# Performance work log

Hardware: AMD Instinct MI355X
Metric: run time of the kernel (lower is better)

## Reference

```python
import jax, jax.numpy as jnp
import numpy as np

N = 100_000      # nodes
E = 1_600_000    # edges (avg degree 16)
D_IN = 64
D_OUT = 64


def setup_inputs() -> dict:
    key = jax.random.key(0)
    k_x, k_row, k_ptr, k_w, k_b = jax.random.split(key, 5)
    x = jax.random.normal(k_x, (N, D_IN), dtype=jnp.float32)
    # CSC graph: row = source node index per edge, colptr = per-target-node edge offsets
    row = jax.random.randint(k_row, (E,), 0, N, dtype=jnp.int32)
    inner = jnp.sort(jax.random.randint(k_ptr, (N - 1,), 0, E, dtype=jnp.int32))
    colptr = jnp.concatenate([jnp.zeros((1,), jnp.int32), inner,
                              jnp.full((1,), E, jnp.int32)])
    # Linear(2*in_channels -> out_channels) weights, torch layout [out, in]
    W = jax.random.normal(k_w, (D_OUT, 2 * D_IN), dtype=jnp.float32) * 0.05
    b = jax.random.normal(k_b, (D_OUT,), dtype=jnp.float32) * 0.05
    return {"x": x, "row": row, "colptr": colptr, "W": W, "b": b}


def reference(x, row, colptr, W, b):
    num_nodes = x.shape[0]
    num_edges = row.shape[0]
    # Recover per-edge target node id from colptr (CSC -> COO col)
    col = jnp.searchsorted(colptr, jnp.arange(num_edges, dtype=colptr.dtype),
                           side='right') - 1  # [E]
    # Mean aggregation of neighbor (source) features onto target nodes
    gathered = x[row]                                             # [E, D_IN]
    summed = jax.ops.segment_sum(gathered, col, num_segments=num_nodes)
    deg = (colptr[1:] - colptr[:-1]).astype(x.dtype)              # [N]
    agg = summed / jnp.clip(deg, 1.0)[:, None]                    # [N, D_IN]
    # SAGEConvAgg output = concat(agg_neighbors, root features); then Linear
    feat = jnp.concatenate([agg, x], axis=-1)                     # [N, 2*D_IN]
    return feat @ W.T + b                                         # [N, D_OUT]
```

## Files before the change

### kernel.cpp

```cpp
#include <hip/hip_runtime.h>

typedef __bf16 bf16x8 __attribute__((ext_vector_type(8)));
typedef float  f32x4  __attribute__((ext_vector_type(4)));

__device__ __forceinline__ unsigned short f2bf(float f) {
  unsigned u = __float_as_uint(f);
  u = u + 0x7fffu + ((u >> 16) & 1u);
  return (unsigned short)(u >> 16);
}
__device__ __forceinline__ float bf2f(unsigned short h) {
  return __uint_as_float(((unsigned)h) << 16);
}

__global__ __launch_bounds__(256) void cvt_bf16(
    const float* __restrict__ x, unsigned short* __restrict__ xb, int total8) {
  int i = blockIdx.x * 256 + threadIdx.x;
  if (i >= total8) return;
  const float4* p = (const float4*)(x + (size_t)i * 8);
  float4 a = p[0], b = p[1];
  union { unsigned short u[8]; uint4 v; } r;
  r.u[0] = f2bf(a.x); r.u[1] = f2bf(a.y); r.u[2] = f2bf(a.z); r.u[3] = f2bf(a.w);
  r.u[4] = f2bf(b.x); r.u[5] = f2bf(b.y); r.u[6] = f2bf(b.z); r.u[7] = f2bf(b.w);
  ((uint4*)xb)[i] = r.v;
}

template <bool BF>
__global__ __launch_bounds__(256) void sage_agg(
    const float* __restrict__ x, const unsigned short* __restrict__ xb,
    const int* __restrict__ row, const int* __restrict__ colptr,
    float* __restrict__ agg, int N) {
  int wid  = blockIdx.x * 4 + (threadIdx.x >> 6);
  int lane = threadIdx.x & 63;
  if (wid >= N) return;
  int s = colptr[wid], e = colptr[wid + 1];
  float acc = 0.0f;
  int t = s;
#define LDX(r) (BF ? bf2f(xb[(size_t)(r) * 64 + lane]) : x[(size_t)(r) * 64 + lane])
  for (; t + 8 <= e; t += 8) {
    int r0 = row[t],     r1 = row[t + 1], r2 = row[t + 2], r3 = row[t + 3];
    int r4 = row[t + 4], r5 = row[t + 5], r6 = row[t + 6], r7 = row[t + 7];
    float v0 = LDX(r0), v1 = LDX(r1), v2 = LDX(r2), v3 = LDX(r3);
    float v4 = LDX(r4), v5 = LDX(r5), v6 = LDX(r6), v7 = LDX(r7);
    acc += ((v0 + v1) + (v2 + v3)) + ((v4 + v5) + (v6 + v7));
  }
  for (; t + 4 <= e; t += 4) {
    int r0 = row[t], r1 = row[t + 1], r2 = row[t + 2], r3 = row[t + 3];
    float v0 = LDX(r0), v1 = LDX(r1), v2 = LDX(r2), v3 = LDX(r3);
    acc += (v0 + v1) + (v2 + v3);
  }
  for (; t < e; ++t) acc += LDX(row[t]);
#undef LDX
  int deg = e - s;
  agg[(size_t)wid * 64 + lane] = (deg > 0) ? (acc / (float)deg) : 0.0f;
}

template <bool BF>
__global__ __launch_bounds__(256) void sage_mm(
    const float* __restrict__ x, const unsigned short* __restrict__ xb,
    const float* __restrict__ W, const float* __restrict__ b,
    float* __restrict__ out, int N) {
  __shared__ unsigned short ft[128][136];
  int tid = threadIdx.x;
  int l = tid & 63, w = tid >> 6;
  int colr = l & 15, kg = l >> 4;
  int n0 = blockIdx.x * 128;
  int rows = N - n0; if (rows > 128) rows = 128;

  bf16x8 bfrag[4][4];
  float bias[4];
  #pragma unroll
  for (int c = 0; c < 4; ++c) {
    bias[c] = b[c * 16 + colr];
    #pragma unroll
    for (int kq = 0; kq < 4; ++kq) {
      const float* wp = W + (size_t)(c * 16 + colr) * 128 + kq * 32 + kg * 8;
      float4 wa = *(const float4*)wp;
      float4 wb = *(const float4*)(wp + 4);
      union { unsigned short u[8]; bf16x8 v; } r;
      r.u[0] = f2bf(wa.x); r.u[1] = f2bf(wa.y); r.u[2] = f2bf(wa.z); r.u[3] = f2bf(wa.w);
      r.u[4] = f2bf(wb.x); r.u[5] = f2bf(wb.y); r.u[6] = f2bf(wb.z); r.u[7] = f2bf(wb.w);
      bfrag[c][kq] = r.v;
    }
  }

  const float* aggsrc = out + (size_t)n0 * 64;
  #pragma unroll
  for (int it = 0; it < 4; ++it) {
    int flat = it * 2048 + tid * 8;
    int n = flat >> 6, k = flat & 63;
    {
      union { unsigned short u[8]; uint4 v; } r;
      if (n < rows) {
        const float4* p = (const float4*)(aggsrc + (size_t)n * 64 + k);
        float4 a = p[0], bb = p[1];
        r.u[0] = f2bf(a.x);  r.u[1] = f2bf(a.y);  r.u[2] = f2bf(a.z);  r.u[3] = f2bf(a.w);
        r.u[4] = f2bf(bb.x); r.u[5] = f2bf(bb.y); r.u[6] = f2bf(bb.z); r.u[7] = f2bf(bb.w);
      } else { r.v = make_uint4(0, 0, 0, 0); }
      *(uint4*)&ft[n][k] = r.v;
    }
    {
      uint4 v;
      if (BF) {
        v = (n < rows) ? *(const uint4*)(xb + ((size_t)(n0 + n) * 64 + k))
                       : make_uint4(0, 0, 0, 0);
      } else {
        union { unsigned short u[8]; uint4 vv; } r;
        if (n < rows) {
          const float4* p = (const float4*)(x + (size_t)(n0 + n) * 64 + k);
          float4 a = p[0], bb = p[1];
          r.u[0] = f2bf(a.x);  r.u[1] = f2bf(a.y);  r.u[2] = f2bf(a.z);  r.u[3] = f2bf(a.w);
          r.u[4] = f2bf(bb.x); r.u[5] = f2bf(bb.y); r.u[6] = f2bf(bb.z); r.u[7] = f2bf(bb.w);
        } else { r.vv = make_uint4(0, 0, 0, 0); }
        v = r.vv;
      }
      *(uint4*)&ft[n][64 + k] = v;
    }
  }
  __syncthreads();

  f32x4 acc[2][4];
  #pragma unroll
  for (int m = 0; m < 2; ++m)
    #pragma unroll
    for (int c = 0; c < 4; ++c)
      acc[m][c] = (f32x4){bias[c], bias[c], bias[c], bias[c]};

  #pragma unroll
  for (int kq = 0; kq < 4; ++kq) {
    bf16x8 a0 = *(const bf16x8*)&ft[w * 32 + colr][kq * 32 + kg * 8];
    bf16x8 a1 = *(const bf16x8*)&ft[w * 32 + 16 + colr][kq * 32 + kg * 8];
    #pragma unroll
    for (int c = 0; c < 4; ++c) {
      acc[0][c] = __builtin_amdgcn_mfma_f32_16x16x32_bf16(a0, bfrag[c][kq], acc[0][c], 0, 0, 0);
      acc[1][c] = __builtin_amdgcn_mfma_f32_16x16x32_bf16(a1, bfrag[c][kq], acc[1][c], 0, 0, 0);
    }
  }

  #pragma unroll
  for (int m = 0; m < 2; ++m) {
    int nodeb = n0 + w * 32 + m * 16 + kg * 4;
    #pragma unroll
    for (int c = 0; c < 4; ++c) {
      #pragma unroll
      for (int r = 0; r < 4; ++r) {
        int node = nodeb + r;
        if (node < N) out[(size_t)node * 64 + c * 16 + colr] = acc[m][c][r];
      }
    }
  }
}

extern "C" void kernel_launch(void* const* d_in, const int* in_sizes, int n_in,
                              void* d_out, int out_size, void* d_ws, size_t ws_size,
                              hipStream_t stream) {
  const float* x      = (const float*)d_in[0];
  const int*   row    = (const int*)d_in[1];
  const int*   colptr = (const int*)d_in[2];
  const float* W      = (const float*)d_in[3];
  const float* b      = (const float*)d_in[4];
  float* out = (float*)d_out;

  int N = in_sizes[0] / 64;
  bool bf = ws_size >= (size_t)N * 64 * sizeof(unsigned short);
  unsigned short* xb = (unsigned short*)d_ws;

  if (bf) {
    int total8 = N * 8;
    cvt_bf16<<<(total8 + 255) / 256, 256, 0, stream>>>(x, xb, total8);
    sage_agg<true><<<(N + 3) / 4, 256, 0, stream>>>(x, xb, row, colptr, out, N);
    sage_mm<true><<<(N + 127) / 128, 256, 0, stream>>>(x, xb, W, b, out, N);
  } else {
    sage_agg<false><<<(N + 3) / 4, 256, 0, stream>>>(x, xb, row, colptr, out, N);
    sage_mm<false><<<(N + 127) / 128, 256, 0, stream>>>(x, xb, W, b, out, N);
  }
}
```

Before: 94.71 us.

## Fuse neighbor aggregation into the MFMA linear kernel via shared memory

Merges the separate aggregation and matmul kernels into one: each wave gathers and averages neighbor features for 32 nodes and writes the bf16 result straight into the shared tile used by the MFMA product. This removes the fp32 round trip of the aggregated features through global memory and one kernel launch. In exchange, the gather runs with far fewer waves (one block per 128 nodes, each wave looping serially over nodes), which reduces the memory-level parallelism available to hide random gather latency. The edge loop is unrolled to 16 to compensate.

```diff
diff --git a/kernel.cpp b/kernel.cpp
--- a/kernel.cpp
+++ b/kernel.cpp
@@ -25,105 +25,79 @@
 }
 
 template <bool BF>
-__global__ __launch_bounds__(256) void sage_agg(
+__global__ __launch_bounds__(256, 4) void sage_fused(
     const float* __restrict__ x, const unsigned short* __restrict__ xb,
     const int* __restrict__ row, const int* __restrict__ colptr,
-    float* __restrict__ agg, int N) {
-  int wid  = blockIdx.x * 4 + (threadIdx.x >> 6);
-  int lane = threadIdx.x & 63;
-  if (wid >= N) return;
-  int s = colptr[wid], e = colptr[wid + 1];
-  float acc = 0.0f;
-  int t = s;
-#define LDX(r) (BF ? bf2f(xb[(size_t)(r) * 64 + lane]) : x[(size_t)(r) * 64 + lane])
-  for (; t + 8 <= e; t += 8) {
-    int r0 = row[t],     r1 = row[t + 1], r2 = row[t + 2], r3 = row[t + 3];
-    int r4 = row[t + 4], r5 = row[t + 5], r6 = row[t + 6], r7 = row[t + 7];
-    float v0 = LDX(r0), v1 = LDX(r1), v2 = LDX(r2), v3 = LDX(r3);
-    float v4 = LDX(r4), v5 = LDX(r5), v6 = LDX(r6), v7 = LDX(r7);
-    acc += ((v0 + v1) + (v2 + v3)) + ((v4 + v5) + (v6 + v7));
-  }
-  for (; t + 4 <= e; t += 4) {
-    int r0 = row[t], r1 = row[t + 1], r2 = row[t + 2], r3 = row[t + 3];
-    float v0 = LDX(r0), v1 = LDX(r1), v2 = LDX(r2), v3 = LDX(r3);
-    acc += (v0 + v1) + (v2 + v3);
-  }
-  for (; t < e; ++t) acc += LDX(row[t]);
-#undef LDX
-  int deg = e - s;
-  agg[(size_t)wid * 64 + lane] = (deg > 0) ? (acc / (float)deg) : 0.0f;
-}
-
-template <bool BF>
-__global__ __launch_bounds__(256) void sage_mm(
-    const float* __restrict__ x, const unsigned short* __restrict__ xb,
-    const float* __restrict__ W, const float* __restrict__ b,
+    const float* __restrict__ W, const float* __restrict__ bias,
     float* __restrict__ out, int N) {
   __shared__ unsigned short ft[128][136];
   int tid = threadIdx.x;
   int l = tid & 63, w = tid >> 6;
-  int colr = l & 15, kg = l >> 4;
   int n0 = blockIdx.x * 128;
   int rows = N - n0; if (rows > 128) rows = 128;
 
-  bf16x8 bfrag[4][4];
-  float bias[4];
-  #pragma unroll
-  for (int c = 0; c < 4; ++c) {
-    bias[c] = b[c * 16 + colr];
-    #pragma unroll
-    for (int kq = 0; kq < 4; ++kq) {
-      const float* wp = W + (size_t)(c * 16 + colr) * 128 + kq * 32 + kg * 8;
-      float4 wa = *(const float4*)wp;
-      float4 wb = *(const float4*)(wp + 4);
-      union { unsigned short u[8]; bf16x8 v; } r;
-      r.u[0] = f2bf(wa.x); r.u[1] = f2bf(wa.y); r.u[2] = f2bf(wa.z); r.u[3] = f2bf(wa.w);
-      r.u[4] = f2bf(wb.x); r.u[5] = f2bf(wb.y); r.u[6] = f2bf(wb.z); r.u[7] = f2bf(wb.w);
-      bfrag[c][kq] = r.v;
+#define LDX(r) (BF ? bf2f(xb[(size_t)(r) * 64 + l]) : x[(size_t)(r) * 64 + l])
+  for (int i = 0; i < 32; ++i) {
+    int node = n0 + w * 32 + i;
+    float acc = 0.0f;
+    int deg = 0;
+    if (node < N) {
+      int s = colptr[node], e = colptr[node + 1];
+      deg = e - s;
+      int t = s;
+      for (; t + 16 <= e; t += 16) {
+        int r0 = row[t], r1 = row[t+1], r2 = row[t+2], r3 = row[t+3];
+        int r4 = row[t+4], r5 = row[t+5], r6 = row[t+6], r7 = row[t+7];
+        int r8 = row[t+8], r9 = row[t+9], r10 = row[t+10], r11 = row[t+11];
+        int r12 = row[t+12], r13 = row[t+13], r14 = row[t+14], r15 = row[t+15];
+        float v0 = LDX(r0),  v1 = LDX(r1),  v2 = LDX(r2),  v3 = LDX(r3);
+        float v4 = LDX(r4),  v5 = LDX(r5),  v6 = LDX(r6),  v7 = LDX(r7);
+        float v8 = LDX(r8),  v9 = LDX(r9),  v10 = LDX(r10), v11 = LDX(r11);
+        float v12 = LDX(r12), v13 = LDX(r13), v14 = LDX(r14), v15 = LDX(r15);
+        acc += (((v0+v1)+(v2+v3)) + ((v4+v5)+(v6+v7)))
+             + (((v8+v9)+(v10+v11)) + ((v12+v13)+(v14+v15)));
+      }
+      for (; t + 4 <= e; t += 4) {
+        int r0 = row[t], r1 = row[t+1], r2 = row[t+2], r3 = row[t+3];
+        float v0 = LDX(r0), v1 = LDX(r1), v2 = LDX(r2), v3 = LDX(r3);
+        acc += (v0 + v1) + (v2 + v3);
+      }
+      for (; t < e; ++t) acc += LDX(row[t]);
     }
+    float scale = (deg > 0) ? (1.0f / (float)deg) : 0.0f;
+    ft[w * 32 + i][l] = f2bf(acc * scale);
   }
+#undef LDX
 
-  const float* aggsrc = out + (size_t)n0 * 64;
   #pragma unroll
   for (int it = 0; it < 4; ++it) {
     int flat = it * 2048 + tid * 8;
     int n = flat >> 6, k = flat & 63;
-    {
-      union { unsigned short u[8]; uint4 v; } r;
-      if (n < rows) {
-        const float4* p = (const float4*)(aggsrc + (size_t)n * 64 + k);
+    uint4 v = make_uint4(0, 0, 0, 0);
+    if (n < rows) {
+      if (BF) {
+        v = *(const uint4*)(xb + ((size_t)(n0 + n) * 64 + k));
+      } else {
+        const float4* p = (const float4*)(x + (size_t)(n0 + n) * 64 + k);
         float4 a = p[0], bb = p[1];
+        union { unsigned short u[8]; uint4 vv; } r;
         r.u[0] = f2bf(a.x);  r.u[1] = f2bf(a.y);  r.u[2] = f2bf(a.z);  r.u[3] = f2bf(a.w);
         r.u[4] = f2bf(bb.x); r.u[5] = f2bf(bb.y); r.u[6] = f2bf(bb.z); r.u[7] = f2bf(bb.w);
-      } else { r.v = make_uint4(0, 0, 0, 0); }
-      *(uint4*)&ft[n][k] = r.v;
-    }
-    {
-      uint4 v;
-      if (BF) {
-        v = (n < rows) ? *(const uint4*)(xb + ((size_t)(n0 + n) * 64 + k))
-                       : make_uint4(0, 0, 0, 0);
-      } else {
-        union { unsigned short u[8]; uint4 vv; } r;
-        if (n < rows) {
-          const float4* p = (const float4*)(x + (size_t)(n0 + n) * 64 + k);
-          float4 a = p[0], bb = p[1];
-          r.u[0] = f2bf(a.x);  r.u[1] = f2bf(a.y);  r.u[2] = f2bf(a.z);  r.u[3] = f2bf(a.w);
-          r.u[4] = f2bf(bb.x); r.u[5] = f2bf(bb.y); r.u[6] = f2bf(bb.z); r.u[7] = f2bf(bb.w);
-        } else { r.vv = make_uint4(0, 0, 0, 0); }
         v = r.vv;
       }
-      *(uint4*)&ft[n][64 + k] = v;
     }
+    *(uint4*)&ft[n][64 + k] = v;
   }
   __syncthreads();
 
+  int colr = l & 15, kg = l >> 4;
   f32x4 acc[2][4];
   #pragma unroll
-  for (int m = 0; m < 2; ++m)
-    #pragma unroll
-    for (int c = 0; c < 4; ++c)
-      acc[m][c] = (f32x4){bias[c], bias[c], bias[c], bias[c]};
+  for (int c = 0; c < 4; ++c) {
+    float bv = bias[c * 16 + colr];
+    acc[0][c] = (f32x4){bv, bv, bv, bv};
+    acc[1][c] = acc[0][c];
+  }
 
   #pragma unroll
   for (int kq = 0; kq < 4; ++kq) {
@@ -131,8 +105,14 @@
     bf16x8 a1 = *(const bf16x8*)&ft[w * 32 + 16 + colr][kq * 32 + kg * 8];
     #pragma unroll
     for (int c = 0; c < 4; ++c) {
-      acc[0][c] = __builtin_amdgcn_mfma_f32_16x16x32_bf16(a0, bfrag[c][kq], acc[0][c], 0, 0, 0);
-      acc[1][c] = __builtin_amdgcn_mfma_f32_16x16x32_bf16(a1, bfrag[c][kq], acc[1][c], 0, 0, 0);
+      const float* wp = W + (size_t)(c * 16 + colr) * 128 + kq * 32 + kg * 8;
+      float4 wa = *(const float4*)wp;
+      float4 wb = *(const float4*)(wp + 4);
+      union { unsigned short u[8]; bf16x8 v; } r;
+      r.u[0] = f2bf(wa.x); r.u[1] = f2bf(wa.y); r.u[2] = f2bf(wa.z); r.u[3] = f2bf(wa.w);
+      r.u[4] = f2bf(wb.x); r.u[5] = f2bf(wb.y); r.u[6] = f2bf(wb.z); r.u[7] = f2bf(wb.w);
+      acc[0][c] = __builtin_amdgcn_mfma_f32_16x16x32_bf16(a0, r.v, acc[0][c], 0, 0, 0);
+      acc[1][c] = __builtin_amdgcn_mfma_f32_16x16x32_bf16(a1, r.v, acc[1][c], 0, 0, 0);
     }
   }
 
@@ -164,13 +144,12 @@
   bool bf = ws_size >= (size_t)N * 64 * sizeof(unsigned short);
   unsigned short* xb = (unsigned short*)d_ws;
 
+  int nb = (N + 127) / 128;
   if (bf) {
     int total8 = N * 8;
     cvt_bf16<<<(total8 + 255) / 256, 256, 0, stream>>>(x, xb, total8);
-    sage_agg<true><<<(N + 3) / 4, 256, 0, stream>>>(x, xb, row, colptr, out, N);
-    sage_mm<true><<<(N + 127) / 128, 256, 0, stream>>>(x, xb, W, b, out, N);
+    sage_fused<true><<<nb, 256, 0, stream>>>(x, xb, row, colptr, W, b, out, N);
   } else {
-    sage_agg<false><<<(N + 3) / 4, 256, 0, stream>>>(x, xb, row, colptr, out, N);
-    sage_mm<false><<<(N + 127) / 128, 256, 0, stream>>>(x, xb, W, b, out, N);
+    sage_fused<false><<<nb, 256, 0, stream>>>(x, xb, row, colptr, W, b, out, N);
   }
 }
```

Result: slower. 119.4 us (+26.1%).
